# Optimization experiments

Hardware: AMD Instinct MI355X
Metric: run time of the kernel (lower is better)

## Reference

```python
import jax, jax.numpy as jnp
import numpy as np

DIM, HEADS, EMB = 768, 16, 1024
DH = DIM // HEADS                 # 48, divisible by 3 for 3D RoPE
T, RES = 3, 24
KT, KH, KW = 3, 5, 5              # neighborhood kernel
MLP = 4 * DIM
EPS = 1e-5


def _ln(x, w=None, b=None):
    m = x.mean(-1, keepdims=True)
    v = x.var(-1, keepdims=True)
    y = (x - m) * jax.lax.rsqrt(v + EPS)
    if w is not None:
        y = y * w + b
    return y


def _rope_cos_sin():
    # 3D axial RoPE: dim_head split into 3 equal chunks (t, h, w axes)
    da = DH // 3
    half = da // 2
    inv = 1.0 / (10000.0 ** (jnp.arange(half, dtype=jnp.float32) * 2.0 / da))
    def ang(n):
        return jnp.arange(n, dtype=jnp.float32)[:, None] * inv[None, :]  # (n, half)
    at, ah, aw = ang(T), ang(RES), ang(RES)
    A = jnp.concatenate([
        jnp.broadcast_to(at[:, None, None, :], (T, RES, RES, half)),
        jnp.broadcast_to(ah[None, :, None, :], (T, RES, RES, half)),
        jnp.broadcast_to(aw[None, None, :, :], (T, RES, RES, half)),
    ], axis=-1).reshape(T * RES * RES, DH // 2)
    return jnp.cos(A), jnp.sin(A)


def _rope(x, cos, sin):  # x: (B, nh, THW, DH); interleaved pair rotation
    x1, x2 = x[..., 0::2], x[..., 1::2]
    o1 = x1 * cos - x2 * sin
    o2 = x1 * sin + x2 * cos
    return jnp.stack([o1, o2], axis=-1).reshape(x.shape)


def _nbr(n, k):
    # NATTEN window: centered, shifted inward at borders (always exactly k neighbors)
    start = jnp.clip(jnp.arange(n) - k // 2, 0, n - k)
    return start[:, None] + jnp.arange(k)  # (n, k)


def setup_inputs():
    key = jax.random.key(0)
    ks = jax.random.split(key, 8)
    r = lambda k, s: jax.random.normal(k, s, dtype=jnp.float32) * 0.02
    return {
        "x": jax.random.normal(ks[0], (T, DIM, RES, RES), dtype=jnp.float32),
        "emb": jax.random.normal(ks[1], (T, EMB), dtype=jnp.float32),
        "w_mod": r(ks[2], (EMB, 2 * DIM)),
        "b_mod": jnp.zeros((2 * DIM,), jnp.float32),
        "qn_w": jnp.ones((DH,), jnp.float32),
        "qn_b": jnp.zeros((DH,), jnp.float32),
        "kn_w": jnp.ones((DH,), jnp.float32),
        "kn_b": jnp.zeros((DH,), jnp.float32),
        "W_fused": r(ks[3], (DIM, 3 * DIM + MLP)),
        "b_fused": jnp.zeros((3 * DIM + MLP,), jnp.float32),
        "W_out": r(ks[4], (DIM, DIM)),
        "W_mlp": r(ks[5], (MLP, DIM)),
        "b_mlp": jnp.zeros((DIM,), jnp.float32),
    }


def reference(x, emb, w_mod, b_mod, qn_w, qn_b, kn_w, kn_b,
              W_fused, b_fused, W_out, W_mlp, b_mlp):
    B = x.shape[0] // T
    H = W = RES
    THW = T * H * W
    x5 = x.reshape(B, T, DIM, H, W)
    skip = jnp.transpose(x5, (0, 1, 3, 4, 2))          # (B,T,H,W,C)
    xf = skip.reshape(B, THW, DIM)
    # conditioning emb repeated over spatial positions
    embr = jnp.repeat(emb.reshape(B, T, EMB)[:, :, None, :], H * W, axis=2)
    embr = embr.reshape(B, THW, EMB)
    # NormalizeWithCond: LayerNorm (no affine) + AdaLN modulation from emb
    mod = jax.nn.silu(embr) @ w_mod + b_mod
    scale, shift = jnp.split(mod, 2, axis=-1)
    h = _ln(xf) * (1.0 + scale) + shift
    # fused QKV + MLP projection
    fused = h @ W_fused + b_fused
    qkv, mlp_h = fused[..., :3 * DIM], fused[..., 3 * DIM:]
    qkv = qkv.reshape(B, THW, 3, HEADS, DH).transpose(2, 0, 3, 1, 4)  # (3,B,nh,THW,d)
    q, k, v = qkv[0], qkv[1], qkv[2]
    q = _ln(q, qn_w, qn_b)
    k = _ln(k, kn_w, kn_b)
    cos, sin = _rope_cos_sin()
    q = _rope(q, cos, sin)
    k = _rope(k, cos, sin)
    q = q.reshape(B, HEADS, T, H, W, DH) * (DH ** -0.5)
    k = k.reshape(B, HEADS, T, H, W, DH)
    v = v.reshape(B, HEADS, T, H, W, DH)
    it, ih, iw = _nbr(T, KT), _nbr(H, KH), _nbr(W, KW)
    def gather(z):  # -> (B,nh,T,KT,H,KH,W,KW,d)
        return z[:, :, it][:, :, :, :, ih][:, :, :, :, :, :, iw]
    kg, vg = gather(k), gather(v)
    attn = jnp.einsum('bnthwd,bntahcwed->bnthwace', q, kg)
    attn = jax.nn.softmax(attn.reshape(B, HEADS, T, H, W, KT * KH * KW), axis=-1)
    attn = attn.reshape(B, HEADS, T, H, W, KT, KH, KW)
    xa = jnp.einsum('bnthwace,bntahcwed->bnthwd', attn, vg)
    xa = jnp.transpose(xa, (0, 2, 3, 4, 1, 5)).reshape(B, T, H, W, DIM)
    y = skip + xa @ W_out
    y = y.reshape(B, THW, DIM) + (jax.nn.silu(mlp_h) @ W_mlp + b_mlp)
    y = jnp.transpose(y.reshape(B, T, H, W, DIM), (0, 1, 4, 2, 3))
    return y.reshape(B * T, DIM, H, W)
```

## Files before the change

### kernel.cpp

```cpp
#include <hip/hip_runtime.h>
#include <hip/hip_bf16.h>
#include <math.h>

#define T_    3
#define RES_  24
#define DIM_  768
#define HEADS_ 16
#define DH_   48
#define EMB_  1024
#define HW_   576
#define THW_  1728
#define MP_   1792
#define MLP_  3072
#define NF_   5376
#define QKV_  2304
#define QK_   1536
#define KTOT_ 3840
#define SPLITK_ 6
#define EPS_  1e-5f

typedef __attribute__((ext_vector_type(8))) short bf16x8;
typedef __attribute__((ext_vector_type(4))) float f32x4;

__device__ __forceinline__ float siluf(float x) { return x / (1.f + expf(-x)); }

__device__ __forceinline__ unsigned short f2bf(float f) {
    __hip_bfloat16 b = __float2bfloat16(f);
    return *reinterpret_cast<unsigned short*>(&b);
}

__device__ __forceinline__ float bf2f(unsigned short u) {
    return __uint_as_float(((unsigned)u) << 16);
}

__device__ __forceinline__ void async_copy16(const void* g, void* l) {
    __builtin_amdgcn_global_load_lds(
        (__attribute__((address_space(1))) void*)g,
        (__attribute__((address_space(3))) void*)l,
        16, 0, 0);
}

__global__ __launch_bounds__(256) void conv_wfused_kernel(
    const float* __restrict__ W, unsigned short* __restrict__ Wt)
{
    __shared__ float tile[32][33];
    int n0 = blockIdx.x * 32;
    int k0 = blockIdx.y * 32;
    int c = threadIdx.x & 31;
    int r = threadIdx.x >> 5;
#pragma unroll
    for (int i = 0; i < 4; ++i)
        tile[r + 8 * i][c] = W[(size_t)(k0 + r + 8 * i) * NF_ + n0 + c];
    __syncthreads();
#pragma unroll
    for (int i = 0; i < 4; ++i)
        Wt[(size_t)(n0 + r + 8 * i) * DIM_ + k0 + c] = f2bf(tile[c][r + 8 * i]);
}

__global__ __launch_bounds__(256) void conv_wcat_kernel(
    const float* __restrict__ W_out, const float* __restrict__ W_mlp,
    unsigned short* __restrict__ Wt)
{
    __shared__ float tile[32][33];
    int k0 = blockIdx.x * 32;
    int n0 = blockIdx.y * 32;
    int c = threadIdx.x & 31;
    int r = threadIdx.x >> 5;
#pragma unroll
    for (int i = 0; i < 4; ++i) {
        int k = k0 + r + 8 * i;
        float v = (k < DIM_) ? W_out[(size_t)k * DIM_ + n0 + c]
                             : W_mlp[(size_t)(k - DIM_) * DIM_ + n0 + c];
        tile[r + 8 * i][c] = v;
    }
    __syncthreads();
#pragma unroll
    for (int i = 0; i < 4; ++i)
        Wt[(size_t)(n0 + r + 8 * i) * KTOT_ + k0 + c] = f2bf(tile[c][r + 8 * i]);
}

__global__ __launch_bounds__(256) void mod_kernel(
    const float* __restrict__ emb, const float* __restrict__ w_mod,
    const float* __restrict__ b_mod, float* __restrict__ mod)
{
    int t = blockIdx.y;
    int chunk = blockIdx.x;
    __shared__ float se[EMB_];
    __shared__ float part[128];
    int tid = threadIdx.x;
    for (int i = tid; i < EMB_; i += 256) {
        float e = emb[t * EMB_ + i];
        se[i] = e / (1.f + expf(-e));
    }
    __syncthreads();
    int r = tid >> 7;
    int c = tid & 127;
    int j = chunk * 128 + c;
    const float* wp = w_mod + j;
    float acc = 0.f;
    for (int e = r * 512; e < r * 512 + 512; ++e)
        acc += se[e] * wp[e * 1536];
    if (r == 1) part[c] = acc;
    __syncthreads();
    if (r == 0)
        mod[t * 1536 + j] = acc + part[c] + b_mod[j];
}

__global__ __launch_bounds__(256) void ln_mod_kernel(
    const float* __restrict__ x, const float* __restrict__ mod,
    unsigned short* __restrict__ h)
{
    int m0 = blockIdx.x * 4;
    int t = m0 / HW_;
    int hw0 = m0 - t * HW_;
    const float* xp = x + (size_t)t * DIM_ * HW_ + hw0;
    int tid = threadIdx.x;
    float4 X0 = *(const float4*)(xp + (size_t)tid * HW_);
    float4 X1 = *(const float4*)(xp + (size_t)(tid + 256) * HW_);
    float4 X2 = *(const float4*)(xp + (size_t)(tid + 512) * HW_);
    float4 sv, sqv;
    sv.x = X0.x + X1.x + X2.x;  sv.y = X0.y + X1.y + X2.y;
    sv.z = X0.z + X1.z + X2.z;  sv.w = X0.w + X1.w + X2.w;
    sqv.x = X0.x*X0.x + X1.x*X1.x + X2.x*X2.x;
    sqv.y = X0.y*X0.y + X1.y*X1.y + X2.y*X2.y;
    sqv.z = X0.z*X0.z + X1.z*X1.z + X2.z*X2.z;
    sqv.w = X0.w*X0.w + X1.w*X1.w + X2.w*X2.w;
#pragma unroll
    for (int off = 32; off > 0; off >>= 1) {
        sv.x += __shfl_xor(sv.x, off, 64);  sv.y += __shfl_xor(sv.y, off, 64);
        sv.z += __shfl_xor(sv.z, off, 64);  sv.w += __shfl_xor(sv.w, off, 64);
        sqv.x += __shfl_xor(sqv.x, off, 64); sqv.y += __shfl_xor(sqv.y, off, 64);
        sqv.z += __shfl_xor(sqv.z, off, 64); sqv.w += __shfl_xor(sqv.w, off, 64);
    }
    __shared__ float4 ssum[4], ssq[4];
    int lane = tid & 63, wid = tid >> 6;
    if (lane == 0) { ssum[wid] = sv; ssq[wid] = sqv; }
    __syncthreads();
    float mean[4], rs[4];
#pragma unroll
    for (int j = 0; j < 4; ++j) {
        float tot  = ((const float*)&ssum[0])[j] + ((const float*)&ssum[1])[j]
                   + ((const float*)&ssum[2])[j] + ((const float*)&ssum[3])[j];
        float totq = ((const float*)&ssq[0])[j] + ((const float*)&ssq[1])[j]
                   + ((const float*)&ssq[2])[j] + ((const float*)&ssq[3])[j];
        float mn = tot * (1.f / 768.f);
        float var = totq * (1.f / 768.f) - mn * mn;
        mean[j] = mn;
        rs[j] = rsqrtf(var + EPS_);
    }
    const float* sc = mod + t * 1536;
    const float* sh = sc + 768;
#pragma unroll
    for (int cc = 0; cc < 3; ++cc) {
        int c = tid + cc * 256;
        float4 X = (cc == 0) ? X0 : (cc == 1) ? X1 : X2;
        float scl = 1.f + sc[c];
        float shf = sh[c];
        const float* Xp = (const float*)&X;
#pragma unroll
        for (int j = 0; j < 4; ++j)
            h[(size_t)(m0 + j) * DIM_ + c] =
                f2bf((Xp[j] - mean[j]) * rs[j] * scl + shf);
    }
}

__global__ __launch_bounds__(256) void gemm1_kernel(
    const unsigned short* __restrict__ A,
    const unsigned short* __restrict__ Bt,
    const float* __restrict__ bias,
    float* __restrict__ qkv,
    unsigned short* __restrict__ vb,
    unsigned short* __restrict__ A2)
{
    const int K = DIM_;
    __shared__ unsigned short As[128 * 32];
    __shared__ unsigned short Bs[128 * 32];
    int tid = threadIdx.x;
    int bm = blockIdx.y * 128;
    int bn = blockIdx.x * 128;
    int wave = tid >> 6, lane = tid & 63;
    int quad = lane >> 4, l16 = lane & 15;
    int wm = (wave & 1) * 64;
    int wn = (wave >> 1) * 64;
    f32x4 acc[4][4] = {};
    int srow = tid >> 2;
    int skk  = (tid & 3) * 8;
    const unsigned short* Ag = A + (size_t)(bm + srow) * K + skk;
    const unsigned short* Bg = Bt + (size_t)(bn + srow) * K + skk;
    unsigned short* la0 = &As[srow * 32 + skk];
    unsigned short* la1 = &As[(srow + 64) * 32 + skk];
    unsigned short* lb0 = &Bs[srow * 32 + skk];
    unsigned short* lb1 = &Bs[(srow + 64) * 32 + skk];
    for (int k0 = 0; k0 < K; k0 += 32) {
        async_copy16(Ag + k0, la0);
        async_copy16(Ag + (size_t)64 * K + k0, la1);
        async_copy16(Bg + k0, lb0);
        async_copy16(Bg + (size_t)64 * K + k0, lb1);
        __syncthreads();
        bf16x8 af[4], bf[4];
#pragma unroll
        for (int mt = 0; mt < 4; ++mt)
            af[mt] = *(const bf16x8*)&As[(wm + mt * 16 + l16) * 32 + quad * 8];
#pragma unroll
        for (int nt = 0; nt < 4; ++nt)
            bf[nt] = *(const bf16x8*)&Bs[(wn + nt * 16 + l16) * 32 + quad * 8];
#pragma unroll
        for (int mt = 0; mt < 4; ++mt)
#pragma unroll
            for (int nt = 0; nt < 4; ++nt)
                acc[mt][nt] = __builtin_amdgcn_mfma_f32_16x16x32_bf16(
                    af[mt], bf[nt], acc[mt][nt], 0, 0, 0);
        __syncthreads();
    }
#pragma unroll
    for (int mt = 0; mt < 4; ++mt) {
#pragma unroll
        for (int nt = 0; nt < 4; ++nt) {
            int gcol = bn + wn + nt * 16 + l16;
            float b = bias[gcol];
#pragma unroll
            for (int r = 0; r < 4; ++r) {
                int grow = bm + wm + mt * 16 + quad * 4 + r;
                if (grow < THW_) {
                    float v = acc[mt][nt][r] + b;
                    if (gcol < QK_)
                        qkv[(size_t)grow * QK_ + gcol] = v;
                    else if (gcol < QKV_)
                        vb[(size_t)grow * DIM_ + (gcol - QK_)] = f2bf(v);
                    else
                        A2[(size_t)grow * KTOT_ + (gcol - QKV_ + DIM_)] = f2bf(siluf(v));
                }
            }
        }
    }
}

__global__ __launch_bounds__(256) void qkln_rope_kernel(
    const float* __restrict__ qkv,
    const float* __restrict__ qn_w, const float* __restrict__ qn_b,
    const float* __restrict__ kn_w, const float* __restrict__ kn_b,
    unsigned short* __restrict__ qb, unsigned short* __restrict__ kb)
{
    int tid = threadIdx.x;
    int lane = tid & 63, wid = tid >> 6;
    int idx = blockIdx.x * 4 + wid;
    int head = idx / THW_;
    int m = idx - head * THW_;
    const float* fp = qkv + (size_t)m * QK_ + head * DH_;
    float qv = 0.f, kv = 0.f;
    if (lane < DH_) { qv = fp[lane]; kv = fp[768 + lane]; }
    float s = qv, sq = qv * qv, sk = kv, sqk = kv * kv;
#pragma unroll
    for (int off = 32; off > 0; off >>= 1) {
        s   += __shfl_xor(s, off, 64);
        sq  += __shfl_xor(sq, off, 64);
        sk  += __shfl_xor(sk, off, 64);
        sqk += __shfl_xor(sqk, off, 64);
    }
    float mq = s  * (1.f / 48.f), vq = sq  * (1.f / 48.f) - mq * mq;
    float mk = sk * (1.f / 48.f), vk = sqk * (1.f / 48.f) - mk * mk;
    float qn = 0.f, kn = 0.f;
    if (lane < DH_) {
        qn = (qv - mq) * rsqrtf(vq + EPS_) * qn_w[lane] + qn_b[lane];
        kn = (kv - mk) * rsqrtf(vk + EPS_) * kn_w[lane] + kn_b[lane];
    }
    int t = m / HW_; int hw = m - t * HW_;
    int hh = hw / RES_; int ww = hw - hh * RES_;
    int i = lane >> 1;
    int grp = i >> 3, j = i & 7;
    float pos = (grp == 0) ? (float)t : (grp == 1) ? (float)hh : (float)ww;
    float invf = exp2f(-1.6609640474436813f * (float)j);
    float ang = pos * invf;
    float cs = cosf(ang), sn = sinf(ang);
    float qp = __shfl_xor(qn, 1, 64);
    float kp = __shfl_xor(kn, 1, 64);
    float qo, ko;
    if ((lane & 1) == 0) { qo = qn * cs - qp * sn; ko = kn * cs - kp * sn; }
    else                 { qo = qp * sn + qn * cs; ko = kp * sn + kn * cs; }
    if (lane < DH_) {
        size_t o = ((size_t)head * THW_ + m) * DH_ + lane;
        qb[o] = f2bf(qo * 0.14433756729740643f);
        kb[o] = f2bf(ko);
    }
}

__global__ __launch_bounds__(256) void attn_kernel(
    const unsigned short* __restrict__ qb, const unsigned short* __restrict__ kb,
    const unsigned short* __restrict__ vb, unsigned short* __restrict__ A2)
{
    __shared__ unsigned short Ks[144 * 72];
    __shared__ unsigned short Vt[48 * 168];
    __shared__ unsigned short Ps[64 * 168];

    int tid = threadIdx.x;
    int lane = tid & 63, wave = tid >> 6;
    int quad = lane >> 4, l16 = lane & 15;

    int head = blockIdx.x / 27;
    int tile = blockIdx.x - head * 27;
    int tt = tile / 9;
    int sp = tile - tt * 9;
    int h0 = (sp / 3) * 8;
    int w0 = (sp - (sp / 3) * 3) * 8;
    int u0h = min(max(h0 - 2, 0), RES_ - 12);
    int u0w = min(max(w0 - 2, 0), RES_ - 12);

    const unsigned short* qbh = qb + (size_t)head * THW_ * DH_;
    const unsigned short* kbh = kb + (size_t)head * THW_ * DH_;
    const unsigned short* vbh = vb + head * DH_;

    for (int i = tid; i < 144 * 24; i += 256) {
        int r = i / 24;
        Ks[r * 72 + 48 + (i - r * 24)] = 0;
    }
    for (int i = tid; i < 48 * 24; i += 256) {
        int r = i / 24;
        Vt[r * 168 + 144 + (i - r * 24)] = 0;
    }
    for (int i = tid; i < 64 * 24; i += 256) {
        int r = i / 24;
        Ps[r * 168 + 144 + (i - r * 24)] = 0;
    }

    int qbase = wave * 16;
    bf16x8 qf0, qf1;
    {
        int g = qbase + l16;
        int qtok = tt * HW_ + (h0 + (g >> 3)) * RES_ + (w0 + (g & 7));
        const unsigned short* qp = qbh + (size_t)qtok * DH_;
        qf0 = *(const bf16x8*)(qp + quad * 8);
        if (quad < 2) qf1 = *(const bf16x8*)(qp + 32 + quad * 8);
        else {
#pragma unroll
            for (int i = 0; i < 8; ++i) qf1[i] = 0;
        }
    }

    int vmask[4];
#pragma unroll
    for (int r = 0; r < 4; ++r) {
        int g = qbase + quad * 4 + r;
        int qh = h0 + (g >> 3), qw = w0 + (g & 7);
        int hs = min(max(qh - 2, 0), RES_ - 5);
        int ws = min(max(qw - 2, 0), RES_ - 5);
        int vm = 0;
#pragma unroll
        for (int nt = 0; nt < 9; ++nt) {
            int kk = nt * 16 + l16;
            int hc = u0h + kk / 12;
            int wc = u0w + kk - (kk / 12) * 12;
            int ok = (hc >= hs) & (hc < hs + 5) & (wc >= ws) & (wc < ws + 5);
            vm |= ok << nt;
        }
        vmask[r] = vm;
    }

    float mrow[4] = {-1e30f, -1e30f, -1e30f, -1e30f};
    float lrow[4] = {};
    f32x4 Oacc[3] = {};

    for (int a = 0; a < T_; ++a) {
        for (int i = tid; i < 144 * 12; i += 256) {
            int kk = i / 12;
            int g = i - kk * 12;
            int hc = u0h + kk / 12;
            int wc = u0w + kk - (kk / 12) * 12;
            int tok = a * HW_ + hc * RES_ + wc;
            ushort4 k4 = *(const ushort4*)(kbh + (size_t)tok * DH_ + 4 * g);
            *(ushort4*)&Ks[kk * 72 + 4 * g] = k4;
            ushort4 v4 = *(const ushort4*)(vbh + (size_t)tok * DIM_ + 4 * g);
            Vt[(4 * g + 0) * 168 + kk] = v4.x;
            Vt[(4 * g + 1) * 168 + kk] = v4.y;
            Vt[(4 * g + 2) * 168 + kk] = v4.z;
            Vt[(4 * g + 3) * 168 + kk] = v4.w;
        }
        __syncthreads();

        f32x4 sc[9];
#pragma unroll
        for (int nt = 0; nt < 9; ++nt) {
            bf16x8 kf0 = *(const bf16x8*)&Ks[(nt * 16 + l16) * 72 + quad * 8];
            bf16x8 kf1 = *(const bf16x8*)&Ks[(nt * 16 + l16) * 72 + 32 + quad * 8];
            f32x4 z = {};
            z = __builtin_amdgcn_mfma_f32_16x16x32_bf16(qf0, kf0, z, 0, 0, 0);
            sc[nt] = __builtin_amdgcn_mfma_f32_16x16x32_bf16(qf1, kf1, z, 0, 0, 0);
        }

        float rmax[4] = {-1e30f, -1e30f, -1e30f, -1e30f};
#pragma unroll
        for (int nt = 0; nt < 9; ++nt)
#pragma unroll
            for (int r = 0; r < 4; ++r) {
                float s = ((vmask[r] >> nt) & 1) ? sc[nt][r] : -1e30f;
                sc[nt][r] = s;
                rmax[r] = fmaxf(rmax[r], s);
            }
#pragma unroll
        for (int off = 1; off < 16; off <<= 1)
#pragma unroll
            for (int r = 0; r < 4; ++r)
                rmax[r] = fmaxf(rmax[r], __shfl_xor(rmax[r], off));
        float alpha[4], rsum[4] = {};
#pragma unroll
        for (int r = 0; r < 4; ++r) {
            float mn = fmaxf(mrow[r], rmax[r]);
            alpha[r] = expf(mrow[r] - mn);
            mrow[r] = mn;
        }
#pragma unroll
        for (int nt = 0; nt < 9; ++nt)
#pragma unroll
            for (int r = 0; r < 4; ++r) {
                float p = expf(sc[nt][r] - mrow[r]);
                rsum[r] += p;
                Ps[(qbase + quad * 4 + r) * 168 + nt * 16 + l16] = f2bf(p);
            }
#pragma unroll
        for (int off = 1; off < 16; off <<= 1)
#pragma unroll
            for (int r = 0; r < 4; ++r)
                rsum[r] += __shfl_xor(rsum[r], off);
#pragma unroll
        for (int r = 0; r < 4; ++r)
            lrow[r] = lrow[r] * alpha[r] + rsum[r];
#pragma unroll
        for (int vt = 0; vt < 3; ++vt)
#pragma unroll
            for (int r = 0; r < 4; ++r)
                Oacc[vt][r] *= alpha[r];

#pragma unroll
        for (int ks = 0; ks < 5; ++ks) {
            bf16x8 pf = *(const bf16x8*)&Ps[(qbase + l16) * 168 + ks * 32 + quad * 8];
#pragma unroll
            for (int vt = 0; vt < 3; ++vt) {
                bf16x8 vf = *(const bf16x8*)&Vt[(vt * 16 + l16) * 168 + ks * 32 + quad * 8];
                Oacc[vt] = __builtin_amdgcn_mfma_f32_16x16x32_bf16(pf, vf, Oacc[vt], 0, 0, 0);
            }
        }
        __syncthreads();
    }

#pragma unroll
    for (int r = 0; r < 4; ++r) {
        int g = qbase + quad * 4 + r;
        int m = tt * HW_ + (h0 + (g >> 3)) * RES_ + (w0 + (g & 7));
        float inv = 1.f / lrow[r];
#pragma unroll
        for (int vt = 0; vt < 3; ++vt) {
            int d = vt * 16 + l16;
            A2[(size_t)m * KTOT_ + head * DH_ + d] = f2bf(Oacc[vt][r] * inv);
        }
    }
}

__global__ __launch_bounds__(256) void gemm2_kernel(
    const unsigned short* __restrict__ A,
    const unsigned short* __restrict__ Bt,
    unsigned short* __restrict__ P)
{
    const int K = KTOT_;
    __shared__ unsigned short As[128 * 32];
    __shared__ unsigned short Bs[128 * 32];
    int tid = threadIdx.x;
    int bm = blockIdx.y * 128;
    int bn = blockIdx.x * 128;
    int ks = blockIdx.z * (KTOT_ / SPLITK_);
    int wave = tid >> 6, lane = tid & 63;
    int quad = lane >> 4, l16 = lane & 15;
    int wm = (wave & 1) * 64;
    int wn = (wave >> 1) * 64;
    f32x4 acc[4][4] = {};
    int srow = tid >> 2;
    int skk  = (tid & 3) * 8;
    const unsigned short* Ag = A + (size_t)(bm + srow) * K + skk;
    const unsigned short* Bg = Bt + (size_t)(bn + srow) * K + skk;
    unsigned short* la0 = &As[srow * 32 + skk];
    unsigned short* la1 = &As[(srow + 64) * 32 + skk];
    unsigned short* lb0 = &Bs[srow * 32 + skk];
    unsigned short* lb1 = &Bs[(srow + 64) * 32 + skk];
    for (int k0 = ks; k0 < ks + KTOT_ / SPLITK_; k0 += 32) {
        async_copy16(Ag + k0, la0);
        async_copy16(Ag + (size_t)64 * K + k0, la1);
        async_copy16(Bg + k0, lb0);
        async_copy16(Bg + (size_t)64 * K + k0, lb1);
        __syncthreads();
        bf16x8 af[4], bf[4];
#pragma unroll
        for (int mt = 0; mt < 4; ++mt)
            af[mt] = *(const bf16x8*)&As[(wm + mt * 16 + l16) * 32 + quad * 8];
#pragma unroll
        for (int nt = 0; nt < 4; ++nt)
            bf[nt] = *(const bf16x8*)&Bs[(wn + nt * 16 + l16) * 32 + quad * 8];
#pragma unroll
        for (int mt = 0; mt < 4; ++mt)
#pragma unroll
            for (int nt = 0; nt < 4; ++nt)
                acc[mt][nt] = __builtin_amdgcn_mfma_f32_16x16x32_bf16(
                    af[mt], bf[nt], acc[mt][nt], 0, 0, 0);
        __syncthreads();
    }
    unsigned short* Pp = P + (size_t)blockIdx.z * MP_ * DIM_;
#pragma unroll
    for (int mt = 0; mt < 4; ++mt) {
#pragma unroll
        for (int nt = 0; nt < 4; ++nt) {
            int gcol = bn + wn + nt * 16 + l16;
#pragma unroll
            for (int r = 0; r < 4; ++r) {
                int grow = bm + wm + mt * 16 + quad * 4 + r;
                if (grow < THW_)
                    Pp[(size_t)grow * DIM_ + gcol] = f2bf(acc[mt][nt][r]);
            }
        }
    }
}

__global__ __launch_bounds__(256) void reduce_out_kernel(
    const unsigned short* __restrict__ P, const float* __restrict__ x,
    const float* __restrict__ b_mlp, float* __restrict__ out)
{
    __shared__ float tile[32][65];
    int bm = blockIdx.x * 64;
    int bn = blockIdx.y * 32;
    int tid = threadIdx.x;
    int t = bm / HW_;
    int hw0 = bm - t * HW_;
    for (int i = tid; i < 512; i += 256) {
        int ml = i >> 3;
        int n4 = (i & 7) * 4;
        float s0 = 0.f, s1 = 0.f, s2 = 0.f, s3 = 0.f;
#pragma unroll
        for (int sI = 0; sI < SPLITK_; ++sI) {
            const unsigned short* pp =
                P + ((size_t)sI * MP_ + bm + ml) * DIM_ + bn + n4;
            ushort4 u = *(const ushort4*)pp;
            s0 += bf2f(u.x); s1 += bf2f(u.y);
            s2 += bf2f(u.z); s3 += bf2f(u.w);
        }
        tile[n4 + 0][ml] = s0;
        tile[n4 + 1][ml] = s1;
        tile[n4 + 2][ml] = s2;
        tile[n4 + 3][ml] = s3;
    }
    __syncthreads();
    for (int i = tid; i < 512; i += 256) {
        int n = i >> 4;
        int ms = (i & 15) * 4;
        int gn = bn + n;
        size_t base = ((size_t)t * DIM_ + gn) * HW_ + hw0 + ms;
        float bv = b_mlp[gn];
        float4 xv = *(const float4*)(x + base);
        float4 o;
        o.x = xv.x + bv + tile[n][ms + 0];
        o.y = xv.y + bv + tile[n][ms + 1];
        o.z = xv.z + bv + tile[n][ms + 2];
        o.w = xv.w + bv + tile[n][ms + 3];
        *(float4*)(out + base) = o;
    }
}

extern "C" void kernel_launch(void* const* d_in, const int* in_sizes, int n_in,
                              void* d_out, int out_size, void* d_ws, size_t ws_size,
                              hipStream_t stream) {
    const float* x       = (const float*)d_in[0];
    const float* emb     = (const float*)d_in[1];
    const float* w_mod   = (const float*)d_in[2];
    const float* b_mod   = (const float*)d_in[3];
    const float* qn_w    = (const float*)d_in[4];
    const float* qn_b    = (const float*)d_in[5];
    const float* kn_w    = (const float*)d_in[6];
    const float* kn_b    = (const float*)d_in[7];
    const float* W_fused = (const float*)d_in[8];
    const float* b_fused = (const float*)d_in[9];
    const float* W_out   = (const float*)d_in[10];
    const float* W_mlp   = (const float*)d_in[11];
    const float* b_mlp   = (const float*)d_in[12];
    float* out = (float*)d_out;

    char* w = (char*)d_ws;
    float* mod = (float*)w;            w += (size_t)4608 * 4;
    float* qkv = (float*)w;            w += (size_t)THW_ * QK_ * 4;
    unsigned short* vb  = (unsigned short*)w;  w += (size_t)THW_ * DIM_ * 2;
    unsigned short* qb  = (unsigned short*)w;  w += (size_t)HEADS_ * THW_ * DH_ * 2;
    unsigned short* kb  = (unsigned short*)w;  w += (size_t)HEADS_ * THW_ * DH_ * 2;
    unsigned short* h   = (unsigned short*)w;  w += (size_t)MP_ * DIM_ * 2;
    unsigned short* A2  = (unsigned short*)w;  w += (size_t)MP_ * KTOT_ * 2;
    unsigned short* Bt1 = (unsigned short*)w;  w += (size_t)NF_ * DIM_ * 2;
    unsigned short* Bt2 = (unsigned short*)w;  w += (size_t)DIM_ * KTOT_ * 2;
    unsigned short* P   = (unsigned short*)w;  w += (size_t)SPLITK_ * MP_ * DIM_ * 2;

    conv_wfused_kernel<<<dim3(NF_ / 32, DIM_ / 32), 256, 0, stream>>>(W_fused, Bt1);
    conv_wcat_kernel<<<dim3(KTOT_ / 32, DIM_ / 32), 256, 0, stream>>>(W_out, W_mlp, Bt2);
    mod_kernel<<<dim3(12, 3), 256, 0, stream>>>(emb, w_mod, b_mod, mod);
    ln_mod_kernel<<<THW_ / 4, 256, 0, stream>>>(x, mod, h);
    gemm1_kernel<<<dim3(NF_ / 128, MP_ / 128), 256, 0, stream>>>(h, Bt1, b_fused, qkv, vb, A2);
    qkln_rope_kernel<<<(HEADS_ * THW_) / 4, 256, 0, stream>>>(qkv, qn_w, qn_b, kn_w, kn_b, qb, kb);
    attn_kernel<<<HEADS_ * 27, 256, 0, stream>>>(qb, kb, vb, A2);
    gemm2_kernel<<<dim3(DIM_ / 128, MP_ / 128, SPLITK_), 256, 0, stream>>>(A2, Bt2, P);
    reduce_out_kernel<<<dim3(THW_ / 64, DIM_ / 32), 256, 0, stream>>>(P, x, b_mlp, out);
}
```

Measured before the change: 238.0 us.

## Double-buffer LDS tiles in both GEMM kernels to overlap loads with MFMA

Both GEMM kernels now keep two LDS stages for the A and B tiles. Each iteration issues the async global-to-LDS copy for the next K-slice into the other buffer, then runs MFMA on the current one, so only one barrier per iteration is needed instead of two. The goal is to hide global load latency behind the matrix math and cut barrier stalls. In exchange, LDS per block doubles to 32 KB, which could lower occupancy. Correctness depends on the barrier waiting for the outstanding async copies.

```diff
diff --git a/kernel.cpp b/kernel.cpp
--- a/kernel.cpp
+++ b/kernel.cpp
@@ -173,8 +173,9 @@
     unsigned short* __restrict__ A2)
 {
     const int K = DIM_;
-    __shared__ unsigned short As[128 * 32];
-    __shared__ unsigned short Bs[128 * 32];
+    const int NI = K / 32;
+    __shared__ unsigned short As[2][128 * 32];
+    __shared__ unsigned short Bs[2][128 * 32];
     int tid = threadIdx.x;
     int bm = blockIdx.y * 128;
     int bn = blockIdx.x * 128;
@@ -187,30 +188,36 @@
     int skk  = (tid & 3) * 8;
     const unsigned short* Ag = A + (size_t)(bm + srow) * K + skk;
     const unsigned short* Bg = Bt + (size_t)(bn + srow) * K + skk;
-    unsigned short* la0 = &As[srow * 32 + skk];
-    unsigned short* la1 = &As[(srow + 64) * 32 + skk];
-    unsigned short* lb0 = &Bs[srow * 32 + skk];
-    unsigned short* lb1 = &Bs[(srow + 64) * 32 + skk];
-    for (int k0 = 0; k0 < K; k0 += 32) {
-        async_copy16(Ag + k0, la0);
-        async_copy16(Ag + (size_t)64 * K + k0, la1);
-        async_copy16(Bg + k0, lb0);
-        async_copy16(Bg + (size_t)64 * K + k0, lb1);
+    int lo0 = srow * 32 + skk;
+    int lo1 = (srow + 64) * 32 + skk;
+    async_copy16(Ag, &As[0][lo0]);
+    async_copy16(Ag + (size_t)64 * K, &As[0][lo1]);
+    async_copy16(Bg, &Bs[0][lo0]);
+    async_copy16(Bg + (size_t)64 * K, &Bs[0][lo1]);
+    for (int i = 0; i < NI; ++i) {
         __syncthreads();
+        if (i + 1 < NI) {
+            int k0 = (i + 1) * 32;
+            int b = (i + 1) & 1;
+            async_copy16(Ag + k0, &As[b][lo0]);
+            async_copy16(Ag + (size_t)64 * K + k0, &As[b][lo1]);
+            async_copy16(Bg + k0, &Bs[b][lo0]);
+            async_copy16(Bg + (size_t)64 * K + k0, &Bs[b][lo1]);
+        }
+        int b = i & 1;
         bf16x8 af[4], bf[4];
 #pragma unroll
         for (int mt = 0; mt < 4; ++mt)
-            af[mt] = *(const bf16x8*)&As[(wm + mt * 16 + l16) * 32 + quad * 8];
+            af[mt] = *(const bf16x8*)&As[b][(wm + mt * 16 + l16) * 32 + quad * 8];
 #pragma unroll
         for (int nt = 0; nt < 4; ++nt)
-            bf[nt] = *(const bf16x8*)&Bs[(wn + nt * 16 + l16) * 32 + quad * 8];
+            bf[nt] = *(const bf16x8*)&Bs[b][(wn + nt * 16 + l16) * 32 + quad * 8];
 #pragma unroll
         for (int mt = 0; mt < 4; ++mt)
 #pragma unroll
             for (int nt = 0; nt < 4; ++nt)
                 acc[mt][nt] = __builtin_amdgcn_mfma_f32_16x16x32_bf16(
                     af[mt], bf[nt], acc[mt][nt], 0, 0, 0);
-        __syncthreads();
     }
 #pragma unroll
     for (int mt = 0; mt < 4; ++mt) {
@@ -460,8 +467,9 @@
     unsigned short* __restrict__ P)
 {
     const int K = KTOT_;
-    __shared__ unsigned short As[128 * 32];
-    __shared__ unsigned short Bs[128 * 32];
+    const int NI = (KTOT_ / SPLITK_) / 32;
+    __shared__ unsigned short As[2][128 * 32];
+    __shared__ unsigned short Bs[2][128 * 32];
     int tid = threadIdx.x;
     int bm = blockIdx.y * 128;
     int bn = blockIdx.x * 128;
@@ -473,32 +481,38 @@
     f32x4 acc[4][4] = {};
     int srow = tid >> 2;
     int skk  = (tid & 3) * 8;
-    const unsigned short* Ag = A + (size_t)(bm + srow) * K + skk;
-    const unsigned short* Bg = Bt + (size_t)(bn + srow) * K + skk;
-    unsigned short* la0 = &As[srow * 32 + skk];
-    unsigned short* la1 = &As[(srow + 64) * 32 + skk];
-    unsigned short* lb0 = &Bs[srow * 32 + skk];
-    unsigned short* lb1 = &Bs[(srow + 64) * 32 + skk];
-    for (int k0 = ks; k0 < ks + KTOT_ / SPLITK_; k0 += 32) {
-        async_copy16(Ag + k0, la0);
-        async_copy16(Ag + (size_t)64 * K + k0, la1);
-        async_copy16(Bg + k0, lb0);
-        async_copy16(Bg + (size_t)64 * K + k0, lb1);
+    const unsigned short* Ag = A + (size_t)(bm + srow) * K + skk + ks;
+    const unsigned short* Bg = Bt + (size_t)(bn + srow) * K + skk + ks;
+    int lo0 = srow * 32 + skk;
+    int lo1 = (srow + 64) * 32 + skk;
+    async_copy16(Ag, &As[0][lo0]);
+    async_copy16(Ag + (size_t)64 * K, &As[0][lo1]);
+    async_copy16(Bg, &Bs[0][lo0]);
+    async_copy16(Bg + (size_t)64 * K, &Bs[0][lo1]);
+    for (int i = 0; i < NI; ++i) {
         __syncthreads();
+        if (i + 1 < NI) {
+            int k0 = (i + 1) * 32;
+            int b = (i + 1) & 1;
+            async_copy16(Ag + k0, &As[b][lo0]);
+            async_copy16(Ag + (size_t)64 * K + k0, &As[b][lo1]);
+            async_copy16(Bg + k0, &Bs[b][lo0]);
+            async_copy16(Bg + (size_t)64 * K + k0, &Bs[b][lo1]);
+        }
+        int b = i & 1;
         bf16x8 af[4], bf[4];
 #pragma unroll
         for (int mt = 0; mt < 4; ++mt)
-            af[mt] = *(const bf16x8*)&As[(wm + mt * 16 + l16) * 32 + quad * 8];
+            af[mt] = *(const bf16x8*)&As[b][(wm + mt * 16 + l16) * 32 + quad * 8];
 #pragma unroll
         for (int nt = 0; nt < 4; ++nt)
-            bf[nt] = *(const bf16x8*)&Bs[(wn + nt * 16 + l16) * 32 + quad * 8];
+            bf[nt] = *(const bf16x8*)&Bs[b][(wn + nt * 16 + l16) * 32 + quad * 8];
 #pragma unroll
         for (int mt = 0; mt < 4; ++mt)
 #pragma unroll
             for (int nt = 0; nt < 4; ++nt)
                 acc[mt][nt] = __builtin_amdgcn_mfma_f32_16x16x32_bf16(
                     af[mt], bf[nt], acc[mt][nt], 0, 0, 0);
-        __syncthreads();
     }
     unsigned short* Pp = P + (size_t)blockIdx.z * MP_ * DIM_;
 #pragma unroll
```

After: 245.4 us. 3.1% more time.
